# Kernel optimization log

Hardware: AMD Instinct MI355X
Metric: run time of the kernel (lower is better)

Reference implementation:

```python
import jax, jax.numpy as jnp
import numpy as np

N_NODES = 50000
N_EDGES = 800000
D_IN = 128
D_HID = 16
N_CLS = 3


def setup_inputs() -> dict:
    key = jax.random.key(0)
    k = jax.random.split(key, 8)
    x = jax.random.normal(k[0], (N_NODES, D_IN), dtype=jnp.float32)
    edge_index = jax.random.randint(k[1], (2, N_EDGES), 0, N_NODES, dtype=jnp.int64)
    # SAGEConv params: lin_l (applied to aggregated neighbors, has bias),
    # lin_r (applied to root node, no bias) -- PyG defaults with mean aggregation.
    s1 = 1.0 / np.sqrt(D_IN)
    s2 = 1.0 / np.sqrt(D_HID)
    W1_l = jax.random.normal(k[2], (D_HID, D_IN), dtype=jnp.float32) * s1
    b1_l = jnp.zeros((D_HID,), dtype=jnp.float32)
    W1_r = jax.random.normal(k[3], (D_HID, D_IN), dtype=jnp.float32) * s1
    W2_l = jax.random.normal(k[4], (N_CLS, D_HID), dtype=jnp.float32) * s2
    b2_l = jnp.zeros((N_CLS,), dtype=jnp.float32)
    W2_r = jax.random.normal(k[5], (N_CLS, D_HID), dtype=jnp.float32) * s2
    return {"x": x, "edge_index": edge_index, "W1_l": W1_l, "b1_l": b1_l,
            "W1_r": W1_r, "W2_l": W2_l, "b2_l": b2_l, "W2_r": W2_r}


def _mean_aggregate(x, src, dst, num_nodes):
    # messages x_j = x[src] scattered to dst, mean-reduced (PyG SAGEConv aggr='mean')
    summed = jax.ops.segment_sum(x[src], dst, num_segments=num_nodes)  # [N, D]
    counts = jax.ops.segment_sum(jnp.ones((src.shape[0],), dtype=x.dtype), dst,
                                 num_segments=num_nodes)
    return summed / jnp.maximum(counts, 1.0)[:, None]


def _sage_conv(x, src, dst, W_l, b_l, W_r, num_nodes):
    agg = _mean_aggregate(x, src, dst, num_nodes)
    return agg @ W_l.T + b_l + x @ W_r.T


def reference(x, edge_index, W1_l, b1_l, W1_r, W2_l, b2_l, W2_r):
    src, dst = edge_index[0], edge_index[1]
    n = x.shape[0]
    h = jax.nn.relu(_sage_conv(x, src, dst, W1_l, b1_l, W1_r, n))
    h = jax.nn.relu(_sage_conv(h, src, dst, W2_l, b2_l, W2_r, n))
    return jax.nn.log_softmax(h, axis=1)
```

## Files before the change

kernel.cpp:

```cpp
#include <hip/hip_runtime.h>
#include <math.h>

#define D_IN 128
#define N_CLS 3
#define NXCD 8
#define CAPU 64

typedef int v4i __attribute__((ext_vector_type(4)));

__global__ __launch_bounds__(128) void lin1_kernel(
    const float* __restrict__ x, const float* __restrict__ W1l,
    const float* __restrict__ W1r, float* __restrict__ y_l,
    float* __restrict__ y_r, int* __restrict__ deg, int n_nodes)
{
    __shared__ float xs[64 * 132];
    __shared__ float ws[32 * 132];
    const int t = threadIdx.x;
    const int node0 = blockIdx.x * 64;

    {
        int i = blockIdx.x * 128 + t;
        if (i < n_nodes) deg[i] = 0;
    }

    for (int m = t; m < (32 * 128) / 4; m += 128) {
        int f = m * 4;
        int row = f >> 7, col = f & 127;
        const float* srcw = (row < 16) ? (W1l + row * 128 + col)
                                       : (W1r + (row - 16) * 128 + col);
        *(float4*)&ws[row * 132 + col] = *(const float4*)srcw;
    }
    for (int m = t; m < (64 * 128) / 4; m += 128) {
        int f = m * 4;
        int row = f >> 7, col = f & 127;
        int node = node0 + row;
        float4 g = make_float4(0.f, 0.f, 0.f, 0.f);
        if (node < n_nodes) g = *(const float4*)(x + (size_t)node * D_IN + col);
        *(float4*)&xs[row * 132 + col] = g;
    }
    __syncthreads();

    const int ng = t >> 3;
    const int og = t & 7;
    float acc[4][4];
    #pragma unroll
    for (int i = 0; i < 4; ++i)
        #pragma unroll
        for (int j = 0; j < 4; ++j) acc[i][j] = 0.f;

    for (int k = 0; k < 128; k += 4) {
        float4 xv[4], wv[4];
        #pragma unroll
        for (int i = 0; i < 4; ++i)
            xv[i] = *(const float4*)&xs[(ng + 16 * i) * 132 + k];
        #pragma unroll
        for (int j = 0; j < 4; ++j)
            wv[j] = *(const float4*)&ws[(og + 8 * j) * 132 + k];
        #pragma unroll
        for (int i = 0; i < 4; ++i)
            #pragma unroll
            for (int j = 0; j < 4; ++j) {
                acc[i][j] = fmaf(xv[i].x, wv[j].x, acc[i][j]);
                acc[i][j] = fmaf(xv[i].y, wv[j].y, acc[i][j]);
                acc[i][j] = fmaf(xv[i].z, wv[j].z, acc[i][j]);
                acc[i][j] = fmaf(xv[i].w, wv[j].w, acc[i][j]);
            }
    }

    #pragma unroll
    for (int i = 0; i < 4; ++i) {
        int node = node0 + ng + 16 * i;
        if (node >= n_nodes) continue;
        #pragma unroll
        for (int j = 0; j < 4; ++j) {
            int col = og + 8 * j;
            if (col < 16) y_l[(size_t)node * 16 + col] = acc[i][j];
            else          y_r[(size_t)node * 16 + (col - 16)] = acc[i][j];
        }
    }
}

__global__ __launch_bounds__(256) void fillxu_kernel(
    const int* __restrict__ src, const int* __restrict__ dstv,
    int* __restrict__ deg, unsigned short* __restrict__ padadj,
    int n_edges, int n8, int n_nodes, int bpx)
{
    const int xg = blockIdx.x & (NXCD - 1);
    const int q  = blockIdx.x >> 3;
    const int lo = xg * n8;
    int hi = lo + n8; if (hi > n_nodes) hi = n_nodes;
    const int stride = bpx * 256;

    const int e4n = n_edges >> 2;
    for (int i = q * 256 + threadIdx.x; i < e4n; i += stride) {
        v4i d4 = __builtin_nontemporal_load((const v4i*)dstv + i);
        v4i s4 = __builtin_nontemporal_load((const v4i*)src + i);
        if (d4.x >= lo && d4.x < hi) {
            int r = atomicAdd(&deg[d4.x], 1);
            if (r < CAPU) padadj[(size_t)d4.x * CAPU + r] = (unsigned short)s4.x;
        }
        if (d4.y >= lo && d4.y < hi) {
            int r = atomicAdd(&deg[d4.y], 1);
            if (r < CAPU) padadj[(size_t)d4.y * CAPU + r] = (unsigned short)s4.y;
        }
        if (d4.z >= lo && d4.z < hi) {
            int r = atomicAdd(&deg[d4.z], 1);
            if (r < CAPU) padadj[(size_t)d4.z * CAPU + r] = (unsigned short)s4.z;
        }
        if (d4.w >= lo && d4.w < hi) {
            int r = atomicAdd(&deg[d4.w], 1);
            if (r < CAPU) padadj[(size_t)d4.w * CAPU + r] = (unsigned short)s4.w;
        }
    }
    if (q == 0 && threadIdx.x < (n_edges & 3)) {
        int e = (e4n << 2) + threadIdx.x;
        int d = dstv[e];
        if (d >= lo && d < hi) {
            int r = atomicAdd(&deg[d], 1);
            if (r < CAPU) padadj[(size_t)d * CAPU + r] = (unsigned short)src[e];
        }
    }
}

__global__ __launch_bounds__(256) void gather1u_kernel(
    const int* __restrict__ deg, const unsigned short* __restrict__ padadj,
    const float* __restrict__ y_l, const float* __restrict__ y_r,
    const float* __restrict__ b1, const float* __restrict__ W2l,
    const float* __restrict__ W2r, float* __restrict__ z_l,
    float* __restrict__ z_r, int n_nodes, int n8)
{
    const int t = threadIdx.x;
    const int c = t & 15;
    const int xg = blockIdx.x & (NXCD - 1);
    const int q = blockIdx.x >> 3;
    const int local = q * 16 + (t >> 4);
    if (local >= n8) return;
    const int n = xg * n8 + local;
    if (n >= n_nodes) return;

    const int dc = deg[n];
    const int dcl = dc < CAPU ? dc : CAPU;
    const unsigned short* ap = padadj + (size_t)n * CAPU;
    float acc = 0.f;
    int j = 0;
    for (; j + 8 <= dcl; j += 8) {
        uint4 v = *(const uint4*)(ap + j);
        int i0 = v.x & 0xFFFF, i1 = v.x >> 16;
        int i2 = v.y & 0xFFFF, i3 = v.y >> 16;
        int i4 = v.z & 0xFFFF, i5 = v.z >> 16;
        int i6 = v.w & 0xFFFF, i7 = v.w >> 16;
        float a0 = y_l[(size_t)i0 * 16 + c];
        float a1 = y_l[(size_t)i1 * 16 + c];
        float a2 = y_l[(size_t)i2 * 16 + c];
        float a3 = y_l[(size_t)i3 * 16 + c];
        float a4 = y_l[(size_t)i4 * 16 + c];
        float a5 = y_l[(size_t)i5 * 16 + c];
        float a6 = y_l[(size_t)i6 * 16 + c];
        float a7 = y_l[(size_t)i7 * 16 + c];
        acc += ((a0 + a1) + (a2 + a3)) + ((a4 + a5) + (a6 + a7));
    }
    for (; j < dcl; ++j) acc += y_l[(size_t)ap[j] * 16 + c];

    float inv = 1.0f / fmaxf((float)dc, 1.0f);
    float h = fmaxf(fmaf(acc, inv, b1[c] + y_r[(size_t)n * 16 + c]), 0.f);

    float zl[N_CLS], zr[N_CLS];
    #pragma unroll
    for (int o = 0; o < N_CLS; ++o) {
        float pl = h * W2l[o * 16 + c];
        float pr = h * W2r[o * 16 + c];
        #pragma unroll
        for (int d = 1; d < 16; d <<= 1) {
            pl += __shfl_xor(pl, d, 64);
            pr += __shfl_xor(pr, d, 64);
        }
        zl[o] = pl; zr[o] = pr;
    }
    if (c == 0) {
        *(float4*)&z_l[(size_t)n * 4] = make_float4(zl[0], zl[1], zl[2], 0.f);
        *(float4*)&z_r[(size_t)n * 4] = make_float4(zr[0], zr[1], zr[2], 0.f);
    }
}

__global__ __launch_bounds__(256) void gather2u_out_kernel(
    const int* __restrict__ deg, const unsigned short* __restrict__ padadj,
    const float* __restrict__ z_l, const float* __restrict__ z_r,
    const float* __restrict__ b2, float* __restrict__ out,
    int n_nodes, int n8)
{
    const int xg = blockIdx.x & (NXCD - 1);
    const int q = blockIdx.x >> 3;
    const int local = q * 256 + threadIdx.x;
    if (local >= n8) return;
    const int n = xg * n8 + local;
    if (n >= n_nodes) return;

    const int dc = deg[n];
    const int dcl = dc < CAPU ? dc : CAPU;
    const unsigned short* ap = padadj + (size_t)n * CAPU;
    float a0 = 0.f, a1 = 0.f, a2 = 0.f;
    int j = 0;
    for (; j + 8 <= dcl; j += 8) {
        uint4 v = *(const uint4*)(ap + j);
        int i0 = v.x & 0xFFFF, i1 = v.x >> 16;
        int i2 = v.y & 0xFFFF, i3 = v.y >> 16;
        int i4 = v.z & 0xFFFF, i5 = v.z >> 16;
        int i6 = v.w & 0xFFFF, i7 = v.w >> 16;
        float4 v0 = *(const float4*)&z_l[(size_t)i0 * 4];
        float4 v1 = *(const float4*)&z_l[(size_t)i1 * 4];
        float4 v2 = *(const float4*)&z_l[(size_t)i2 * 4];
        float4 v3 = *(const float4*)&z_l[(size_t)i3 * 4];
        float4 v4 = *(const float4*)&z_l[(size_t)i4 * 4];
        float4 v5 = *(const float4*)&z_l[(size_t)i5 * 4];
        float4 v6 = *(const float4*)&z_l[(size_t)i6 * 4];
        float4 v7 = *(const float4*)&z_l[(size_t)i7 * 4];
        a0 += ((v0.x + v1.x) + (v2.x + v3.x)) + ((v4.x + v5.x) + (v6.x + v7.x));
        a1 += ((v0.y + v1.y) + (v2.y + v3.y)) + ((v4.y + v5.y) + (v6.y + v7.y));
        a2 += ((v0.z + v1.z) + (v2.z + v3.z)) + ((v4.z + v5.z) + (v6.z + v7.z));
    }
    for (; j < dcl; ++j) {
        float4 v = *(const float4*)&z_l[(size_t)ap[j] * 4];
        a0 += v.x; a1 += v.y; a2 += v.z;
    }
    float inv = 1.0f / fmaxf((float)dc, 1.0f);
    float4 r = *(const float4*)&z_r[(size_t)n * 4];
    float v0 = fmaxf(fmaf(a0, inv, b2[0] + r.x), 0.f);
    float v1 = fmaxf(fmaf(a1, inv, b2[1] + r.y), 0.f);
    float v2 = fmaxf(fmaf(a2, inv, b2[2] + r.z), 0.f);
    float m = fmaxf(fmaxf(v0, v1), v2);
    float s = expf(v0 - m) + expf(v1 - m) + expf(v2 - m);
    float lse = m + logf(s);
    out[(size_t)n * 3 + 0] = v0 - lse;
    out[(size_t)n * 3 + 1] = v1 - lse;
    out[(size_t)n * 3 + 2] = v2 - lse;
}


__global__ __launch_bounds__(256) void fillx_kernel(
    const int* __restrict__ src, const int* __restrict__ dst,
    int* __restrict__ deg, int* __restrict__ padadj,
    int n_edges, int cap, int n8, int n_nodes, int bpx)
{
    const int xg = blockIdx.x & (NXCD - 1);
    const int q  = blockIdx.x >> 3;
    const int lo = xg * n8;
    int hi = lo + n8; if (hi > n_nodes) hi = n_nodes;
    const int stride = bpx * 256;

    const int e4n = n_edges >> 2;
    for (int i = q * 256 + threadIdx.x; i < e4n; i += stride) {
        int4 d4 = *(const int4*)&dst[i * 4];
        if (d4.x >= lo && d4.x < hi) {
            int r = atomicAdd(&deg[d4.x], 1);
            if (r < cap) padadj[(size_t)d4.x * cap + r] = src[i * 4 + 0];
        }
        if (d4.y >= lo && d4.y < hi) {
            int r = atomicAdd(&deg[d4.y], 1);
            if (r < cap) padadj[(size_t)d4.y * cap + r] = src[i * 4 + 1];
        }
        if (d4.z >= lo && d4.z < hi) {
            int r = atomicAdd(&deg[d4.z], 1);
            if (r < cap) padadj[(size_t)d4.z * cap + r] = src[i * 4 + 2];
        }
        if (d4.w >= lo && d4.w < hi) {
            int r = atomicAdd(&deg[d4.w], 1);
            if (r < cap) padadj[(size_t)d4.w * cap + r] = src[i * 4 + 3];
        }
    }
    if (q == 0 && threadIdx.x < (n_edges & 3)) {
        int e = (e4n << 2) + threadIdx.x;
        int d = dst[e];
        if (d >= lo && d < hi) {
            int r = atomicAdd(&deg[d], 1);
            if (r < cap) padadj[(size_t)d * cap + r] = src[e];
        }
    }
}

__global__ __launch_bounds__(256) void gather1x_kernel(
    const int* __restrict__ deg, const int* __restrict__ padadj,
    const float* __restrict__ y_l, const float* __restrict__ y_r,
    const float* __restrict__ b1, const float* __restrict__ W2l,
    const float* __restrict__ W2r, float* __restrict__ z_l,
    float* __restrict__ z_r, int n_nodes, int cap, int n8)
{
    const int t = threadIdx.x;
    const int c = t & 15;
    const int xg = blockIdx.x & (NXCD - 1);
    const int q = blockIdx.x >> 3;
    const int local = q * 16 + (t >> 4);
    if (local >= n8) return;
    const int n = xg * n8 + local;
    if (n >= n_nodes) return;

    const int dc = deg[n];
    const int* ap = padadj + (size_t)n * cap;
    float acc = 0.f;
    int j = 0;
    for (; j + 4 <= dc; j += 4) {
        int4 s4 = *(const int4*)(ap + j);
        float a0 = y_l[(size_t)s4.x * 16 + c];
        float a1 = y_l[(size_t)s4.y * 16 + c];
        float a2 = y_l[(size_t)s4.z * 16 + c];
        float a3 = y_l[(size_t)s4.w * 16 + c];
        acc += (a0 + a1) + (a2 + a3);
    }
    for (; j < dc; ++j) acc += y_l[(size_t)ap[j] * 16 + c];

    float inv = 1.0f / fmaxf((float)dc, 1.0f);
    float h = fmaxf(fmaf(acc, inv, b1[c] + y_r[(size_t)n * 16 + c]), 0.f);

    float zl[N_CLS], zr[N_CLS];
    #pragma unroll
    for (int o = 0; o < N_CLS; ++o) {
        float pl = h * W2l[o * 16 + c];
        float pr = h * W2r[o * 16 + c];
        #pragma unroll
        for (int d = 1; d < 16; d <<= 1) {
            pl += __shfl_xor(pl, d, 64);
            pr += __shfl_xor(pr, d, 64);
        }
        zl[o] = pl; zr[o] = pr;
    }
    if (c == 0) {
        *(float4*)&z_l[(size_t)n * 4] = make_float4(zl[0], zl[1], zl[2], 0.f);
        *(float4*)&z_r[(size_t)n * 4] = make_float4(zr[0], zr[1], zr[2], 0.f);
    }
}

__global__ __launch_bounds__(256) void gather2x_out_kernel(
    const int* __restrict__ deg, const int* __restrict__ padadj,
    const float* __restrict__ z_l, const float* __restrict__ z_r,
    const float* __restrict__ b2, float* __restrict__ out,
    int n_nodes, int cap, int n8)
{
    const int xg = blockIdx.x & (NXCD - 1);
    const int q = blockIdx.x >> 3;
    const int local = q * 256 + threadIdx.x;
    if (local >= n8) return;
    const int n = xg * n8 + local;
    if (n >= n_nodes) return;

    const int dc = deg[n];
    const int* ap = padadj + (size_t)n * cap;
    float a0 = 0.f, a1 = 0.f, a2 = 0.f;
    int j = 0;
    for (; j + 4 <= dc; j += 4) {
        int4 s4 = *(const int4*)(ap + j);
        float4 v0 = *(const float4*)&z_l[(size_t)s4.x * 4];
        float4 v1 = *(const float4*)&z_l[(size_t)s4.y * 4];
        float4 v2 = *(const float4*)&z_l[(size_t)s4.z * 4];
        float4 v3 = *(const float4*)&z_l[(size_t)s4.w * 4];
        a0 += (v0.x + v1.x) + (v2.x + v3.x);
        a1 += (v0.y + v1.y) + (v2.y + v3.y);
        a2 += (v0.z + v1.z) + (v2.z + v3.z);
    }
    for (; j < dc; ++j) {
        float4 v = *(const float4*)&z_l[(size_t)ap[j] * 4];
        a0 += v.x; a1 += v.y; a2 += v.z;
    }
    float inv = 1.0f / fmaxf((float)dc, 1.0f);
    float4 r = *(const float4*)&z_r[(size_t)n * 4];
    float v0 = fmaxf(fmaf(a0, inv, b2[0] + r.x), 0.f);
    float v1 = fmaxf(fmaf(a1, inv, b2[1] + r.y), 0.f);
    float v2 = fmaxf(fmaf(a2, inv, b2[2] + r.z), 0.f);
    float m = fmaxf(fmaxf(v0, v1), v2);
    float s = expf(v0 - m) + expf(v1 - m) + expf(v2 - m);
    float lse = m + logf(s);
    out[(size_t)n * 3 + 0] = v0 - lse;
    out[(size_t)n * 3 + 1] = v1 - lse;
    out[(size_t)n * 3 + 2] = v2 - lse;
}

extern "C" void kernel_launch(void* const* d_in, const int* in_sizes, int n_in,
                              void* d_out, int out_size, void* d_ws, size_t ws_size,
                              hipStream_t stream)
{
    const float* x   = (const float*)d_in[0];
    const int*   ei  = (const int*)d_in[1];
    const float* W1l = (const float*)d_in[2];
    const float* b1  = (const float*)d_in[3];
    const float* W1r = (const float*)d_in[4];
    const float* W2l = (const float*)d_in[5];
    const float* b2  = (const float*)d_in[6];
    const float* W2r = (const float*)d_in[7];

    const int N = in_sizes[0] / D_IN;
    const int E = in_sizes[1] / 2;
    const int* srcI = ei;
    const int* dstI = ei + E;

    float* fws  = (float*)d_ws;
    float* y_l  = fws;
    float* y_r  = y_l + (size_t)N * 16;
    float* z_l  = y_r + (size_t)N * 16;
    float* z_r  = z_l + (size_t)N * 4;
    int*   iws  = (int*)(z_r + (size_t)N * 4);

    const int n8 = (N + NXCD - 1) / NXCD;
    const int bpx = 128;

    const size_t need_u = 160ULL * N + 4ULL * N + 2ULL * CAPU * N;

    int* deg = iws;
    lin1_kernel<<<(N + 63) / 64, 128, 0, stream>>>(x, W1l, W1r, y_l, y_r, deg, N);

    if (N < 65536 && ws_size >= need_u) {
        unsigned short* padadj = (unsigned short*)(deg + N);

        fillxu_kernel<<<NXCD * bpx, 256, 0, stream>>>(srcI, dstI, deg, padadj,
                                                      E, n8, N, bpx);
        const int g1b = (n8 + 15) / 16;
        gather1u_kernel<<<NXCD * g1b, 256, 0, stream>>>(deg, padadj, y_l, y_r,
                                                        b1, W2l, W2r,
                                                        z_l, z_r, N, n8);
        const int g2b = (n8 + 255) / 256;
        gather2u_out_kernel<<<NXCD * g2b, 256, 0, stream>>>(deg, padadj,
                                                            z_l, z_r, b2,
                                                            (float*)d_out, N, n8);
    } else {
        int CAP = 64;
        if (ws_size < 160ULL * N + 4ULL * N + 256ULL * N) CAP = 48;
        int* padadj = deg + N;

        fillx_kernel<<<NXCD * bpx, 256, 0, stream>>>(srcI, dstI, deg, padadj,
                                                     E, CAP, n8, N, bpx);
        const int g1b = (n8 + 15) / 16;
        gather1x_kernel<<<NXCD * g1b, 256, 0, stream>>>(deg, padadj, y_l, y_r,
                                                        b1, W2l, W2r,
                                                        z_l, z_r, N, CAP, n8);
        const int g2b = (n8 + 255) / 256;
        gather2x_out_kernel<<<NXCD * g2b, 256, 0, stream>>>(deg, padadj,
                                                            z_l, z_r, b2,
                                                            (float*)d_out, N, CAP, n8);
    }
}
```

Before: 96.46 us.

## Replace per-node padded adjacency with block-binned edge buckets and shared-memory aggregation

Replaces the global-atomic per-node padded adjacency build with a two-level binning scheme. Each of 256 edge-chunk blocks uses shared-memory atomics to bin edges into 128-node buckets, with a per-cell cap of 32. The two gather kernels then process one bucket per block and accumulate neighbor features with shared-memory atomics, computing degree counts on the fly. This removes global atomics and scattered adjacency writes, but adds LDS atomic contention, lower parallelism (one block per bucket, about 391 blocks), and the risk of silently dropping edges when a cell overflows its cap.

```diff
diff --git a/kernel.cpp b/kernel.cpp
--- a/kernel.cpp
+++ b/kernel.cpp
@@ -4,9 +4,10 @@
 #define D_IN 128
 #define N_CLS 3
 #define NXCD 8
-#define CAPU 64
-
-typedef int v4i __attribute__((ext_vector_type(4)));
+#define BSH  7
+#define BND  128
+#define BINB 256
+#define CAP  32
 
 __global__ __launch_bounds__(128) void lin1_kernel(
     const float* __restrict__ x, const float* __restrict__ W1l,
@@ -18,7 +19,7 @@
     const int t = threadIdx.x;
     const int node0 = blockIdx.x * 64;
 
-    {
+    if (deg) {
         int i = blockIdx.x * 128 + t;
         if (i < n_nodes) deg[i] = 0;
     }
@@ -80,159 +81,153 @@
     }
 }
 
-__global__ __launch_bounds__(256) void fillxu_kernel(
+__global__ __launch_bounds__(256) void binc_kernel(
     const int* __restrict__ src, const int* __restrict__ dstv,
-    int* __restrict__ deg, unsigned short* __restrict__ padadj,
-    int n_edges, int n8, int n_nodes, int bpx)
-{
-    const int xg = blockIdx.x & (NXCD - 1);
-    const int q  = blockIdx.x >> 3;
-    const int lo = xg * n8;
-    int hi = lo + n8; if (hi > n_nodes) hi = n_nodes;
-    const int stride = bpx * 256;
-
-    const int e4n = n_edges >> 2;
-    for (int i = q * 256 + threadIdx.x; i < e4n; i += stride) {
-        v4i d4 = __builtin_nontemporal_load((const v4i*)dstv + i);
-        v4i s4 = __builtin_nontemporal_load((const v4i*)src + i);
-        if (d4.x >= lo && d4.x < hi) {
-            int r = atomicAdd(&deg[d4.x], 1);
-            if (r < CAPU) padadj[(size_t)d4.x * CAPU + r] = (unsigned short)s4.x;
-        }
-        if (d4.y >= lo && d4.y < hi) {
-            int r = atomicAdd(&deg[d4.y], 1);
-            if (r < CAPU) padadj[(size_t)d4.y * CAPU + r] = (unsigned short)s4.y;
-        }
-        if (d4.z >= lo && d4.z < hi) {
-            int r = atomicAdd(&deg[d4.z], 1);
-            if (r < CAPU) padadj[(size_t)d4.z * CAPU + r] = (unsigned short)s4.z;
-        }
-        if (d4.w >= lo && d4.w < hi) {
-            int r = atomicAdd(&deg[d4.w], 1);
-            if (r < CAPU) padadj[(size_t)d4.w * CAPU + r] = (unsigned short)s4.w;
-        }
-    }
-    if (q == 0 && threadIdx.x < (n_edges & 3)) {
-        int e = (e4n << 2) + threadIdx.x;
-        int d = dstv[e];
-        if (d >= lo && d < hi) {
-            int r = atomicAdd(&deg[d], 1);
-            if (r < CAPU) padadj[(size_t)d * CAPU + r] = (unsigned short)src[e];
-        }
-    }
-}
-
-__global__ __launch_bounds__(256) void gather1u_kernel(
-    const int* __restrict__ deg, const unsigned short* __restrict__ padadj,
+    unsigned int* __restrict__ region, int* __restrict__ cntmat,
+    int e4n, int n_edges, int nb)
+{
+    __shared__ int cur[512];
+    const int blk = blockIdx.x;
+    const int t = threadIdx.x;
+    for (int k = t; k < nb; k += 256) cur[k] = 0;
+    __syncthreads();
+
+    const int chunk = (e4n + BINB - 1) / BINB;
+    int i0 = blk * chunk;
+    int i1 = i0 + chunk; if (i1 > e4n) i1 = e4n;
+    for (int i = i0 + t; i < i1; i += 256) {
+        int4 d4 = *(const int4*)&dstv[i * 4];
+        int4 s4 = *(const int4*)&src[i * 4];
+        int b, r;
+        b = d4.x >> BSH; r = atomicAdd(&cur[b], 1);
+        if (r < CAP) region[((size_t)b * BINB + blk) * CAP + r] =
+            ((unsigned)(d4.x & (BND - 1)) << 16) | (unsigned)s4.x;
+        b = d4.y >> BSH; r = atomicAdd(&cur[b], 1);
+        if (r < CAP) region[((size_t)b * BINB + blk) * CAP + r] =
+            ((unsigned)(d4.y & (BND - 1)) << 16) | (unsigned)s4.y;
+        b = d4.z >> BSH; r = atomicAdd(&cur[b], 1);
+        if (r < CAP) region[((size_t)b * BINB + blk) * CAP + r] =
+            ((unsigned)(d4.z & (BND - 1)) << 16) | (unsigned)s4.z;
+        b = d4.w >> BSH; r = atomicAdd(&cur[b], 1);
+        if (r < CAP) region[((size_t)b * BINB + blk) * CAP + r] =
+            ((unsigned)(d4.w & (BND - 1)) << 16) | (unsigned)s4.w;
+    }
+    if (blk == 0 && t < (n_edges & 3)) {
+        int e = (e4n << 2) + t;
+        int d = dstv[e], s = src[e];
+        int b = d >> BSH;
+        int r = atomicAdd(&cur[b], 1);
+        if (r < CAP) region[((size_t)b * BINB) * CAP + r] =
+            ((unsigned)(d & (BND - 1)) << 16) | (unsigned)s;
+    }
+    __syncthreads();
+    for (int k = t; k < nb; k += 256) {
+        int v = cur[k]; if (v > CAP) v = CAP;
+        cntmat[(size_t)blk * nb + k] = v;
+    }
+}
+
+__global__ __launch_bounds__(256) void g1b_kernel(
+    const unsigned int* __restrict__ region, const int* __restrict__ cntmat,
     const float* __restrict__ y_l, const float* __restrict__ y_r,
     const float* __restrict__ b1, const float* __restrict__ W2l,
     const float* __restrict__ W2r, float* __restrict__ z_l,
-    float* __restrict__ z_r, int n_nodes, int n8)
-{
+    float* __restrict__ z_r, int* __restrict__ deg, int n_nodes, int nb)
+{
+    __shared__ float agg[BND * 16];
+    __shared__ int cnt[BND];
     const int t = threadIdx.x;
     const int c = t & 15;
-    const int xg = blockIdx.x & (NXCD - 1);
-    const int q = blockIdx.x >> 3;
-    const int local = q * 16 + (t >> 4);
-    if (local >= n8) return;
-    const int n = xg * n8 + local;
-    if (n >= n_nodes) return;
-
-    const int dc = deg[n];
-    const int dcl = dc < CAPU ? dc : CAPU;
-    const unsigned short* ap = padadj + (size_t)n * CAPU;
-    float acc = 0.f;
-    int j = 0;
-    for (; j + 8 <= dcl; j += 8) {
-        uint4 v = *(const uint4*)(ap + j);
-        int i0 = v.x & 0xFFFF, i1 = v.x >> 16;
-        int i2 = v.y & 0xFFFF, i3 = v.y >> 16;
-        int i4 = v.z & 0xFFFF, i5 = v.z >> 16;
-        int i6 = v.w & 0xFFFF, i7 = v.w >> 16;
-        float a0 = y_l[(size_t)i0 * 16 + c];
-        float a1 = y_l[(size_t)i1 * 16 + c];
-        float a2 = y_l[(size_t)i2 * 16 + c];
-        float a3 = y_l[(size_t)i3 * 16 + c];
-        float a4 = y_l[(size_t)i4 * 16 + c];
-        float a5 = y_l[(size_t)i5 * 16 + c];
-        float a6 = y_l[(size_t)i6 * 16 + c];
-        float a7 = y_l[(size_t)i7 * 16 + c];
-        acc += ((a0 + a1) + (a2 + a3)) + ((a4 + a5) + (a6 + a7));
-    }
-    for (; j < dcl; ++j) acc += y_l[(size_t)ap[j] * 16 + c];
-
-    float inv = 1.0f / fmaxf((float)dc, 1.0f);
-    float h = fmaxf(fmaf(acc, inv, b1[c] + y_r[(size_t)n * 16 + c]), 0.f);
-
-    float zl[N_CLS], zr[N_CLS];
-    #pragma unroll
-    for (int o = 0; o < N_CLS; ++o) {
-        float pl = h * W2l[o * 16 + c];
-        float pr = h * W2r[o * 16 + c];
-        #pragma unroll
-        for (int d = 1; d < 16; d <<= 1) {
-            pl += __shfl_xor(pl, d, 64);
-            pr += __shfl_xor(pr, d, 64);
-        }
-        zl[o] = pl; zr[o] = pr;
-    }
-    if (c == 0) {
-        *(float4*)&z_l[(size_t)n * 4] = make_float4(zl[0], zl[1], zl[2], 0.f);
-        *(float4*)&z_r[(size_t)n * 4] = make_float4(zr[0], zr[1], zr[2], 0.f);
-    }
-}
-
-__global__ __launch_bounds__(256) void gather2u_out_kernel(
-    const int* __restrict__ deg, const unsigned short* __restrict__ padadj,
+    const int g = t >> 4;
+    const int bucket = blockIdx.x;
+
+    for (int k = t; k < BND * 16; k += 256) agg[k] = 0.f;
+    if (t < BND) cnt[t] = 0;
+    __syncthreads();
+
+    for (int cell = g; cell < BINB; cell += 16) {
+        int m = cntmat[(size_t)cell * nb + bucket];
+        const unsigned int* ep = region + ((size_t)bucket * BINB + cell) * CAP;
+        for (int j = 0; j < m; ++j) {
+            unsigned int e = ep[j];
+            int d = e >> 16;
+            int s = e & 0xFFFF;
+            atomicAdd(&agg[d * 16 + c], y_l[(size_t)s * 16 + c]);
+            if (c == 0) atomicAdd(&cnt[d], 1);
+        }
+    }
+    __syncthreads();
+
+    for (int it = 0; it < BND / 16; ++it) {
+        int local = g + 16 * it;
+        int n = (bucket << BSH) + local;
+        if (n >= n_nodes) continue;
+        float inv = 1.0f / fmaxf((float)cnt[local], 1.0f);
+        float h = fmaxf(fmaf(agg[local * 16 + c], inv,
+                             b1[c] + y_r[(size_t)n * 16 + c]), 0.f);
+        float zl[N_CLS], zr[N_CLS];
+        #pragma unroll
+        for (int o = 0; o < N_CLS; ++o) {
+            float pl = h * W2l[o * 16 + c];
+            float pr = h * W2r[o * 16 + c];
+            #pragma unroll
+            for (int d = 1; d < 16; d <<= 1) {
+                pl += __shfl_xor(pl, d, 64);
+                pr += __shfl_xor(pr, d, 64);
+            }
+            zl[o] = pl; zr[o] = pr;
+        }
+        if (c == 0) {
+            *(float4*)&z_l[(size_t)n * 4] = make_float4(zl[0], zl[1], zl[2], 0.f);
+            *(float4*)&z_r[(size_t)n * 4] = make_float4(zr[0], zr[1], zr[2], 0.f);
+            deg[n] = cnt[local];
+        }
+    }
+}
+
+__global__ __launch_bounds__(256) void g2b_kernel(
+    const unsigned int* __restrict__ region, const int* __restrict__ cntmat,
     const float* __restrict__ z_l, const float* __restrict__ z_r,
-    const float* __restrict__ b2, float* __restrict__ out,
-    int n_nodes, int n8)
-{
-    const int xg = blockIdx.x & (NXCD - 1);
-    const int q = blockIdx.x >> 3;
-    const int local = q * 256 + threadIdx.x;
-    if (local >= n8) return;
-    const int n = xg * n8 + local;
-    if (n >= n_nodes) return;
-
-    const int dc = deg[n];
-    const int dcl = dc < CAPU ? dc : CAPU;
-    const unsigned short* ap = padadj + (size_t)n * CAPU;
-    float a0 = 0.f, a1 = 0.f, a2 = 0.f;
-    int j = 0;
-    for (; j + 8 <= dcl; j += 8) {
-        uint4 v = *(const uint4*)(ap + j);
-        int i0 = v.x & 0xFFFF, i1 = v.x >> 16;
-        int i2 = v.y & 0xFFFF, i3 = v.y >> 16;
-        int i4 = v.z & 0xFFFF, i5 = v.z >> 16;
-        int i6 = v.w & 0xFFFF, i7 = v.w >> 16;
-        float4 v0 = *(const float4*)&z_l[(size_t)i0 * 4];
-        float4 v1 = *(const float4*)&z_l[(size_t)i1 * 4];
-        float4 v2 = *(const float4*)&z_l[(size_t)i2 * 4];
-        float4 v3 = *(const float4*)&z_l[(size_t)i3 * 4];
-        float4 v4 = *(const float4*)&z_l[(size_t)i4 * 4];
-        float4 v5 = *(const float4*)&z_l[(size_t)i5 * 4];
-        float4 v6 = *(const float4*)&z_l[(size_t)i6 * 4];
-        float4 v7 = *(const float4*)&z_l[(size_t)i7 * 4];
-        a0 += ((v0.x + v1.x) + (v2.x + v3.x)) + ((v4.x + v5.x) + (v6.x + v7.x));
-        a1 += ((v0.y + v1.y) + (v2.y + v3.y)) + ((v4.y + v5.y) + (v6.y + v7.y));
-        a2 += ((v0.z + v1.z) + (v2.z + v3.z)) + ((v4.z + v5.z) + (v6.z + v7.z));
-    }
-    for (; j < dcl; ++j) {
-        float4 v = *(const float4*)&z_l[(size_t)ap[j] * 4];
-        a0 += v.x; a1 += v.y; a2 += v.z;
-    }
-    float inv = 1.0f / fmaxf((float)dc, 1.0f);
-    float4 r = *(const float4*)&z_r[(size_t)n * 4];
-    float v0 = fmaxf(fmaf(a0, inv, b2[0] + r.x), 0.f);
-    float v1 = fmaxf(fmaf(a1, inv, b2[1] + r.y), 0.f);
-    float v2 = fmaxf(fmaf(a2, inv, b2[2] + r.z), 0.f);
-    float m = fmaxf(fmaxf(v0, v1), v2);
-    float s = expf(v0 - m) + expf(v1 - m) + expf(v2 - m);
-    float lse = m + logf(s);
-    out[(size_t)n * 3 + 0] = v0 - lse;
-    out[(size_t)n * 3 + 1] = v1 - lse;
-    out[(size_t)n * 3 + 2] = v2 - lse;
+    const int* __restrict__ deg, const float* __restrict__ b2,
+    float* __restrict__ out, int n_nodes, int nb)
+{
+    __shared__ float agg2[BND * 4];
+    const int t = threadIdx.x;
+    const int c = t & 3;
+    const int g = t >> 2;
+    const int bucket = blockIdx.x;
+
+    for (int k = t; k < BND * 4; k += 256) agg2[k] = 0.f;
+    __syncthreads();
+
+    for (int cell = g; cell < BINB; cell += 64) {
+        int m = cntmat[(size_t)cell * nb + bucket];
+        const unsigned int* ep = region + ((size_t)bucket * BINB + cell) * CAP;
+        for (int j = 0; j < m; ++j) {
+            unsigned int e = ep[j];
+            int d = e >> 16;
+            int s = e & 0xFFFF;
+            if (c < 3) atomicAdd(&agg2[d * 4 + c], z_l[(size_t)s * 4 + c]);
+        }
+    }
+    __syncthreads();
+
+    if (t < BND) {
+        int n = (bucket << BSH) + t;
+        if (n < n_nodes) {
+            float inv = 1.0f / fmaxf((float)deg[n], 1.0f);
+            float4 r = *(const float4*)&z_r[(size_t)n * 4];
+            float v0 = fmaxf(fmaf(agg2[t * 4 + 0], inv, b2[0] + r.x), 0.f);
+            float v1 = fmaxf(fmaf(agg2[t * 4 + 1], inv, b2[1] + r.y), 0.f);
+            float v2 = fmaxf(fmaf(agg2[t * 4 + 2], inv, b2[2] + r.z), 0.f);
+            float m = fmaxf(fmaxf(v0, v1), v2);
+            float s = expf(v0 - m) + expf(v1 - m) + expf(v2 - m);
+            float lse = m + logf(s);
+            out[(size_t)n * 3 + 0] = v0 - lse;
+            out[(size_t)n * 3 + 1] = v1 - lse;
+            out[(size_t)n * 3 + 2] = v2 - lse;
+        }
+    }
 }
 
 
@@ -397,41 +392,44 @@
     float* z_r  = z_l + (size_t)N * 4;
     int*   iws  = (int*)(z_r + (size_t)N * 4);
 
-    const int n8 = (N + NXCD - 1) / NXCD;
-    const int bpx = 128;
-
-    const size_t need_u = 160ULL * N + 4ULL * N + 2ULL * CAPU * N;
-
-    int* deg = iws;
-    lin1_kernel<<<(N + 63) / 64, 128, 0, stream>>>(x, W1l, W1r, y_l, y_r, deg, N);
-
-    if (N < 65536 && ws_size >= need_u) {
-        unsigned short* padadj = (unsigned short*)(deg + N);
-
-        fillxu_kernel<<<NXCD * bpx, 256, 0, stream>>>(srcI, dstI, deg, padadj,
-                                                      E, n8, N, bpx);
-        const int g1b = (n8 + 15) / 16;
-        gather1u_kernel<<<NXCD * g1b, 256, 0, stream>>>(deg, padadj, y_l, y_r,
-                                                        b1, W2l, W2r,
-                                                        z_l, z_r, N, n8);
-        const int g2b = (n8 + 255) / 256;
-        gather2u_out_kernel<<<NXCD * g2b, 256, 0, stream>>>(deg, padadj,
-                                                            z_l, z_r, b2,
-                                                            (float*)d_out, N, n8);
+    const int NB = (N + BND - 1) >> BSH;
+    const size_t need_main = 160ULL * N + 4ULL * N +
+        4ULL * (size_t)BINB * NB + 4ULL * (size_t)NB * BINB * CAP;
+
+    if (N < 65536 && ws_size >= need_main) {
+        int* deg = iws;
+        int* cntmat = deg + N;
+        unsigned int* region = (unsigned int*)(cntmat + (size_t)BINB * NB);
+
+        const int e4n = E >> 2;
+
+        lin1_kernel<<<(N + 63) / 64, 128, 0, stream>>>(x, W1l, W1r, y_l, y_r,
+                                                       nullptr, N);
+        binc_kernel<<<BINB, 256, 0, stream>>>(srcI, dstI, region, cntmat,
+                                              e4n, E, NB);
+        g1b_kernel<<<NB, 256, 0, stream>>>(region, cntmat, y_l, y_r, b1,
+                                           W2l, W2r, z_l, z_r, deg, N, NB);
+        g2b_kernel<<<NB, 256, 0, stream>>>(region, cntmat, z_l, z_r, deg, b2,
+                                           (float*)d_out, N, NB);
     } else {
-        int CAP = 64;
-        if (ws_size < 160ULL * N + 4ULL * N + 256ULL * N) CAP = 48;
+        const int n8 = (N + NXCD - 1) / NXCD;
+        const int bpx = 128;
+        int CAPF = 64;
+        if (ws_size < 160ULL * N + 4ULL * N + 256ULL * N) CAPF = 48;
+        int* deg    = iws;
         int* padadj = deg + N;
 
+        lin1_kernel<<<(N + 63) / 64, 128, 0, stream>>>(x, W1l, W1r, y_l, y_r,
+                                                       deg, N);
         fillx_kernel<<<NXCD * bpx, 256, 0, stream>>>(srcI, dstI, deg, padadj,
-                                                     E, CAP, n8, N, bpx);
-        const int g1b = (n8 + 15) / 16;
-        gather1x_kernel<<<NXCD * g1b, 256, 0, stream>>>(deg, padadj, y_l, y_r,
-                                                        b1, W2l, W2r,
-                                                        z_l, z_r, N, CAP, n8);
-        const int g2b = (n8 + 255) / 256;
-        gather2x_out_kernel<<<NXCD * g2b, 256, 0, stream>>>(deg, padadj,
-                                                            z_l, z_r, b2,
-                                                            (float*)d_out, N, CAP, n8);
-    }
-}
+                                                     E, CAPF, n8, N, bpx);
+        const int g1b_ = (n8 + 15) / 16;
+        gather1x_kernel<<<NXCD * g1b_, 256, 0, stream>>>(deg, padadj, y_l, y_r,
+                                                         b1, W2l, W2r,
+                                                         z_l, z_r, N, CAPF, n8);
+        const int g2b_ = (n8 + 255) / 256;
+        gather2x_out_kernel<<<NXCD * g2b_, 256, 0, stream>>>(deg, padadj,
+                                                             z_l, z_r, b2,
+                                                             (float*)d_out, N, CAPF, n8);
+    }
+}
```

After: 167.8 us. 74.0% more time.
